# Kernel optimization log

Hardware: AMD Instinct MI355X
Metric: run time of the kernel (lower is better)

The kernel has to match this reference:

```python
import jax, jax.numpy as jnp
import numpy as np

N_NODES = 50000
N_EDGES = 800000
D_IN = 1024
D_OUT = 256
LEAKY_SLOPE = 0.01  # F.leaky_relu default


def setup_inputs() -> dict:
    key = jax.random.key(0)
    k_x, k_w, k_b, k_src, k_dst, k_ew, k_norm = jax.random.split(key, 7)
    x = jax.random.normal(k_x, (N_NODES, D_IN), dtype=jnp.float32)
    # xavier_uniform-style scale for the weight
    limit = np.sqrt(6.0 / (D_IN + D_OUT)).astype(np.float32)
    weight = jax.random.uniform(k_w, (D_IN, D_OUT), dtype=jnp.float32, minval=-limit, maxval=limit)
    stdv = 1.0 / np.sqrt(D_OUT)
    bias = jax.random.uniform(k_b, (D_OUT,), dtype=jnp.float32, minval=-stdv, maxval=stdv)
    src = jax.random.randint(k_src, (N_EDGES,), 0, N_NODES, dtype=jnp.int64)
    dst = jax.random.randint(k_dst, (N_EDGES,), 0, N_NODES, dtype=jnp.int64)
    edge_index = jnp.stack([src, dst], axis=0)  # [2, E]
    edge_weight = jax.random.uniform(k_ew, (N_EDGES,), dtype=jnp.float32)
    norm = jax.random.uniform(k_norm, (N_NODES, 1), dtype=jnp.float32) + 0.5  # avoid div-by-~0
    return {"x": x, "weight": weight, "bias": bias, "edge_index": edge_index,
            "edge_weight": edge_weight, "norm": norm}


def reference(x, weight, bias, edge_index, edge_weight, norm):
    # support = input @ W            [N, D_OUT]
    support = x @ weight
    src = edge_index[0]
    dst = edge_index[1]
    # spmm(adj, support): out[i] = sum_{e: dst_e == i} w_e * support[src_e]
    msgs = support[src] * edge_weight[:, None]            # [E, D_OUT]
    out = jax.ops.segment_sum(msgs, dst, num_segments=x.shape[0])  # [N, D_OUT]
    out = out / norm + bias
    return jax.nn.leaky_relu(out, negative_slope=LEAKY_SLOPE)
```

## Files before the change

kernel.cpp:

```cpp
#include <hip/hip_runtime.h>
#include <hip/hip_bf16.h>

#define N_NODES 50000
#define N_EDGES 800000
#define D_IN    1024
#define D_OUT   256
#define CAP     64
#define LEAKY   0.01f

typedef __attribute__((ext_vector_type(8))) short bf16x8;
typedef __attribute__((ext_vector_type(4))) float f32x4;
typedef __attribute__((ext_vector_type(4))) int   i32x4;
typedef unsigned short u16;

__device__ __forceinline__ u16 f2bfu(float f) {
  uint32_t x = __float_as_uint(f);
  uint32_t r = (x + 0x7FFFu + ((x >> 16) & 1u)) >> 16;
  return (u16)r;
}
__device__ __forceinline__ float bfu2f(u16 u) {
  return __uint_as_float(((uint32_t)u) << 16);
}
__device__ __forceinline__ int swz(int b) { return b ^ (((b >> 7) & 7) << 4); }

__device__ __forceinline__ void gll16(const void* g, void* l) {
  __builtin_amdgcn_global_load_lds(
      (const __attribute__((address_space(1))) uint32_t*)g,
      (__attribute__((address_space(3))) uint32_t*)l, 16, 0, 0);
}

__global__ __launch_bounds__(256) void wconv_kernel(const float* __restrict__ w,
                                                    char* __restrict__ img,
                                                    int* __restrict__ deg) {
  const int t   = blockIdx.x * 256 + threadIdx.x;
  if (t < N_NODES) deg[t] = 0;
  const int t2 = t + 32768;
  if (t2 < N_NODES) deg[t2] = 0;

  const int n   = t & 255;
  const int kc  = (t >> 8) * 8;
  const int kt  = kc >> 6;
  const int kin = kc & 63;
  bf16x8 v;
#pragma unroll
  for (int i = 0; i < 8; ++i) v[i] = (short)f2bfu(w[(size_t)(kc + i) * D_OUT + n]);
  *(bf16x8*)(img + kt * 32768 + swz(n * 128 + kin * 2)) = v;
}

#define BM 64
#define BK 64
#define KSTEPS (D_IN / BK)
#define GEMM_BLOCKS ((N_NODES + BM - 1) / BM)
#define BUILD_BLOCKS 64

__global__ __launch_bounds__(512) void gemm_build_kernel(
    const float* __restrict__ x, const char* __restrict__ img,
    u16* __restrict__ support,
    const int* __restrict__ ei, const float* __restrict__ ew,
    int* __restrict__ deg, int2* __restrict__ csr) {
  __shared__ u16 Wbuf[3][16384];
  __shared__ u16 Xbuf[3][4096];

  if (blockIdx.x < BUILD_BLOCKS) {
    const int t0 = blockIdx.x * 512 + threadIdx.x;
    for (int e = t0; e < N_EDGES; e += BUILD_BLOCKS * 512) {
      const int src = ei[e];
      const int dst = ei[N_EDGES + e];
      const float w = ew[e];
      const int slot = atomicAdd(&deg[dst], 1);
      if (slot < CAP) csr[dst * CAP + slot] = make_int2(src, __float_as_int(w));
    }
    return;
  }

  const int tid  = threadIdx.x;
  const int lane = tid & 63;
  const int wid  = tid >> 6;
  const int wn   = wid & 3;
  const int wm   = wid >> 2;
  const int l15  = lane & 15;
  const int l16  = lane >> 4;
  const int m0   = (blockIdx.x - BUILD_BLOCKS) * BM;

  f32x4 acc[4][2];
#pragma unroll
  for (int i = 0; i < 4; ++i)
#pragma unroll
    for (int j = 0; j < 2; ++j) acc[i][j] = (f32x4)0.0f;

  const int xrow = tid >> 3;
  const int xk8  = (tid & 7) * 8;
  const int xrg  = min(m0 + xrow, N_NODES - 1);
  const float* xp = x + (size_t)xrg * D_IN + xk8;
  const int xw_off = swz(xrow * 128 + xk8 * 2);

  int a_off[2][4], b_off[2][2];
#pragma unroll
  for (int ks = 0; ks < 2; ++ks) {
#pragma unroll
    for (int i = 0; i < 4; ++i)
      a_off[ks][i] = swz((wn * 64 + i * 16 + l15) * 128 + ks * 64 + l16 * 16);
#pragma unroll
    for (int j = 0; j < 2; ++j)
      b_off[ks][j] = swz((wm * 32 + j * 16 + l15) * 128 + ks * 64 + l16 * 16);
  }

  float4 xr[3][2];

#define XLOAD(set, tile) do {                                              \
    const int kcl_ = min((tile), KSTEPS - 1);                              \
    xr[set][0] = *(const float4*)(xp + kcl_ * BK);                         \
    xr[set][1] = *(const float4*)(xp + kcl_ * BK + 4);                     \
  } while (0)

#define WSTAGE(buf, tile) do {                                             \
    const int kcl_ = min((tile), KSTEPS - 1);                              \
    _Pragma("unroll")                                                      \
    for (int r_ = 0; r_ < 4; ++r_)                                         \
      gll16(img + kcl_ * 32768 + r_ * 8192 + tid * 16,                     \
            (char*)&Wbuf[buf][0] + r_ * 8192 + tid * 16);                  \
  } while (0)

#define XCVT(set, buf) do {                                                \
    bf16x8 xv_;                                                            \
    xv_[0] = (short)f2bfu(xr[set][0].x); xv_[1] = (short)f2bfu(xr[set][0].y); \
    xv_[2] = (short)f2bfu(xr[set][0].z); xv_[3] = (short)f2bfu(xr[set][0].w); \
    xv_[4] = (short)f2bfu(xr[set][1].x); xv_[5] = (short)f2bfu(xr[set][1].y); \
    xv_[6] = (short)f2bfu(xr[set][1].z); xv_[7] = (short)f2bfu(xr[set][1].w); \
    *(bf16x8*)((char*)&Xbuf[buf][0] + xw_off) = xv_;                       \
  } while (0)

#define MFMA_TILE(buf) do {                                                \
    _Pragma("unroll")                                                      \
    for (int ks_ = 0; ks_ < 2; ++ks_) {                                    \
      bf16x8 af_[4], bf_[2];                                               \
      _Pragma("unroll")                                                    \
      for (int i_ = 0; i_ < 4; ++i_)                                       \
        af_[i_] = *(const bf16x8*)((const char*)&Wbuf[buf][0] + a_off[ks_][i_]); \
      _Pragma("unroll")                                                    \
      for (int j_ = 0; j_ < 2; ++j_)                                       \
        bf_[j_] = *(const bf16x8*)((const char*)&Xbuf[buf][0] + b_off[ks_][j_]); \
      _Pragma("unroll")                                                    \
      for (int i_ = 0; i_ < 4; ++i_)                                       \
        _Pragma("unroll")                                                  \
        for (int j_ = 0; j_ < 2; ++j_)                                     \
          acc[i_][j_] = __builtin_amdgcn_mfma_f32_16x16x32_bf16(           \
              af_[i_], bf_[j_], acc[i_][j_], 0, 0, 0);                     \
    }                                                                      \
  } while (0)

#define SYNC_COUNTED() do {                                                \
    asm volatile("s_waitcnt vmcnt(6)" ::: "memory");                       \
    __builtin_amdgcn_sched_barrier(0);                                     \
    asm volatile("s_waitcnt lgkmcnt(0)" ::: "memory");                     \
    __builtin_amdgcn_s_barrier();                                          \
  } while (0)

#define BODY(bc, kt) do {                                                  \
    XLOAD((bc + 2) % 3, (kt) + 2);                                         \
    WSTAGE((bc + 2) % 3, (kt) + 2);                                        \
    MFMA_TILE(bc);                                                         \
    XCVT((bc + 1) % 3, (bc + 1) % 3);                                      \
    SYNC_COUNTED();                                                        \
  } while (0)

  XLOAD(0, 0);
  WSTAGE(0, 0);
  XLOAD(1, 1);
  WSTAGE(1, 1);
  XCVT(0, 0);
  SYNC_COUNTED();

  for (int kt = 0; kt < KSTEPS - 1; kt += 3) {
    BODY(0, kt);
    BODY(1, kt + 1);
    BODY(2, kt + 2);
  }
  MFMA_TILE(0);

#undef XLOAD
#undef WSTAGE
#undef XCVT
#undef MFMA_TILE
#undef SYNC_COUNTED
#undef BODY

#pragma unroll
  for (int j = 0; j < 2; ++j) {
    const int m = m0 + wm * 32 + j * 16 + l15;
    if (m < N_NODES) {
#pragma unroll
      for (int i = 0; i < 4; ++i) {
        const int n = wn * 64 + i * 16 + l16 * 4;
        ushort4 o;
        o.x = f2bfu(acc[i][j][0]);
        o.y = f2bfu(acc[i][j][1]);
        o.z = f2bfu(acc[i][j][2]);
        o.w = f2bfu(acc[i][j][3]);
        *(ushort4*)&support[(size_t)m * D_OUT + n] = o;
      }
    }
  }
}

__global__ __launch_bounds__(256) void agg_kernel(const u16* __restrict__ support,
                                                  const int* __restrict__ deg,
                                                  const int2* __restrict__ csr,
                                                  const float* __restrict__ norm,
                                                  const float* __restrict__ bias,
                                                  float* __restrict__ out) {
  const int lane = threadIdx.x & 63;
  const int wid  = threadIdx.x >> 6;
  const int node = blockIdx.x * 4 + wid;
  const int d    = min(deg[node], CAP);
  const int cb   = node * CAP;
  const int ch   = lane * 4;

  float a0 = 0.f, a1 = 0.f, a2 = 0.f, a3 = 0.f;
  int s = 0;

  for (; s + 16 <= d; s += 16) {
    i32x4 q[8];
#pragma unroll
    for (int i = 0; i < 8; ++i)
      q[i] = __builtin_nontemporal_load((const i32x4*)&csr[cb + s + 2 * i]);
    ushort4 v[16];
#pragma unroll
    for (int i = 0; i < 8; ++i) {
      v[2 * i]     = *(const ushort4*)&support[(size_t)q[i][0] * D_OUT + ch];
      v[2 * i + 1] = *(const ushort4*)&support[(size_t)q[i][2] * D_OUT + ch];
    }
#pragma unroll
    for (int i = 0; i < 8; ++i) {
      const float wa = __int_as_float(q[i][1]);
      const float wb = __int_as_float(q[i][3]);
      a0 = fmaf(wa, bfu2f(v[2 * i].x), a0);
      a1 = fmaf(wa, bfu2f(v[2 * i].y), a1);
      a2 = fmaf(wa, bfu2f(v[2 * i].z), a2);
      a3 = fmaf(wa, bfu2f(v[2 * i].w), a3);
      a0 = fmaf(wb, bfu2f(v[2 * i + 1].x), a0);
      a1 = fmaf(wb, bfu2f(v[2 * i + 1].y), a1);
      a2 = fmaf(wb, bfu2f(v[2 * i + 1].z), a2);
      a3 = fmaf(wb, bfu2f(v[2 * i + 1].w), a3);
    }
  }

  for (; s + 8 <= d; s += 8) {
    i32x4 q[4];
#pragma unroll
    for (int i = 0; i < 4; ++i)
      q[i] = __builtin_nontemporal_load((const i32x4*)&csr[cb + s + 2 * i]);
    ushort4 v[8];
#pragma unroll
    for (int i = 0; i < 4; ++i) {
      v[2 * i]     = *(const ushort4*)&support[(size_t)q[i][0] * D_OUT + ch];
      v[2 * i + 1] = *(const ushort4*)&support[(size_t)q[i][2] * D_OUT + ch];
    }
#pragma unroll
    for (int i = 0; i < 4; ++i) {
      const float wa = __int_as_float(q[i][1]);
      const float wb = __int_as_float(q[i][3]);
      a0 = fmaf(wa, bfu2f(v[2 * i].x), a0);
      a1 = fmaf(wa, bfu2f(v[2 * i].y), a1);
      a2 = fmaf(wa, bfu2f(v[2 * i].z), a2);
      a3 = fmaf(wa, bfu2f(v[2 * i].w), a3);
      a0 = fmaf(wb, bfu2f(v[2 * i + 1].x), a0);
      a1 = fmaf(wb, bfu2f(v[2 * i + 1].y), a1);
      a2 = fmaf(wb, bfu2f(v[2 * i + 1].z), a2);
      a3 = fmaf(wb, bfu2f(v[2 * i + 1].w), a3);
    }
  }

  for (; s < d; ++s) {
    const int2  e   = csr[cb + s];
    const float wgt = __int_as_float(e.y);
    const ushort4 v = *(const ushort4*)&support[(size_t)e.x * D_OUT + ch];
    a0 = fmaf(wgt, bfu2f(v.x), a0);
    a1 = fmaf(wgt, bfu2f(v.y), a1);
    a2 = fmaf(wgt, bfu2f(v.z), a2);
    a3 = fmaf(wgt, bfu2f(v.w), a3);
  }

  const float rn = 1.0f / norm[node];
  const float4 b = *(const float4*)&bias[ch];
  float o0 = fmaf(a0, rn, b.x);
  float o1 = fmaf(a1, rn, b.y);
  float o2 = fmaf(a2, rn, b.z);
  float o3 = fmaf(a3, rn, b.w);
  o0 = o0 > 0.f ? o0 : o0 * LEAKY;
  o1 = o1 > 0.f ? o1 : o1 * LEAKY;
  o2 = o2 > 0.f ? o2 : o2 * LEAKY;
  o3 = o3 > 0.f ? o3 : o3 * LEAKY;
  f32x4 ov;
  ov[0] = o0; ov[1] = o1; ov[2] = o2; ov[3] = o3;
  __builtin_nontemporal_store(ov, (f32x4*)&out[(size_t)node * D_OUT + ch]);
}

extern "C" void kernel_launch(void* const* d_in, const int* in_sizes, int n_in,
                              void* d_out, int out_size, void* d_ws, size_t ws_size,
                              hipStream_t stream) {
  const float* x    = (const float*)d_in[0];
  const float* w    = (const float*)d_in[1];
  const float* bias = (const float*)d_in[2];
  const int*   ei   = (const int*)d_in[3];
  const float* ew   = (const float*)d_in[4];
  const float* norm = (const float*)d_in[5];
  float* out = (float*)d_out;

  char* ws = (char*)d_ws;
  u16*   support = (u16*)  (ws);
  char*  img     =         (ws + 25600000);
  int2*  csr     = (int2*) (ws + 26124288);
  int*   deg     = (int*)  (ws + 51724288);

  wconv_kernel<<<128, 256, 0, stream>>>(w, img, deg);
  gemm_build_kernel<<<BUILD_BLOCKS + GEMM_BLOCKS, 512, 0, stream>>>(
      x, img, support, ei, ew, deg, csr);
  agg_kernel<<<N_NODES / 4, 256, 0, stream>>>(support, deg, csr, norm, bias, out);
}
```

Baseline: 168.4 us.

## Enlarge GEMM tile to 256 rows with BK=32 and pairwise-packed swizzled LDS layout

The fused GEMM+CSR-build kernel now gives each block 256 node rows and splits the K dimension into 32-wide steps instead of 64-row blocks with 64-wide steps. Each wave holds a larger 128x64 accumulator tile (8x4 MFMA fragments). The weight image and the LDS buffers use a new packed, swizzled address mapping for the half-width K tiles, and the x loads are marked nontemporal. The bigger tile cuts how often the weight matrix is re-read across blocks and raises MFMA work per LDS read, at the cost of far more accumulator registers, fewer GEMM blocks, a different pipeline phase order and fewer edge-build blocks.

```diff
diff --git a/kernel.cpp b/kernel.cpp
--- a/kernel.cpp
+++ b/kernel.cpp
@@ -22,6 +22,9 @@
   return __uint_as_float(((uint32_t)u) << 16);
 }
 __device__ __forceinline__ int swz(int b) { return b ^ (((b >> 7) & 7) << 4); }
+__device__ __forceinline__ int paddr(int r, int c) {
+  return swz(((r) >> 1) * 128 + ((r) & 1) * 64 + (c));
+}
 
 __device__ __forceinline__ void gll16(const void* g, void* l) {
   __builtin_amdgcn_global_load_lds(
@@ -32,34 +35,32 @@
 __global__ __launch_bounds__(256) void wconv_kernel(const float* __restrict__ w,
                                                     char* __restrict__ img,
                                                     int* __restrict__ deg) {
-  const int t   = blockIdx.x * 256 + threadIdx.x;
+  const int t = blockIdx.x * 256 + threadIdx.x;
   if (t < N_NODES) deg[t] = 0;
   const int t2 = t + 32768;
   if (t2 < N_NODES) deg[t2] = 0;
 
   const int n   = t & 255;
   const int kc  = (t >> 8) * 8;
-  const int kt  = kc >> 6;
-  const int kin = kc & 63;
+  const int kt  = kc >> 5;
+  const int kin = kc & 31;
   bf16x8 v;
 #pragma unroll
   for (int i = 0; i < 8; ++i) v[i] = (short)f2bfu(w[(size_t)(kc + i) * D_OUT + n]);
-  *(bf16x8*)(img + kt * 32768 + swz(n * 128 + kin * 2)) = v;
-}
-
-#define BM 64
-#define BK 64
-#define KSTEPS (D_IN / BK)
-#define GEMM_BLOCKS ((N_NODES + BM - 1) / BM)
-#define BUILD_BLOCKS 64
+  *(bf16x8*)(img + kt * 16384 + paddr(n, kin * 2)) = v;
+}
+
+#define BMg 256
+#define GEMM_BLOCKS ((N_NODES + BMg - 1) / BMg)
+#define BUILD_BLOCKS 60
 
 __global__ __launch_bounds__(512) void gemm_build_kernel(
     const float* __restrict__ x, const char* __restrict__ img,
     u16* __restrict__ support,
     const int* __restrict__ ei, const float* __restrict__ ew,
     int* __restrict__ deg, int2* __restrict__ csr) {
-  __shared__ u16 Wbuf[3][16384];
-  __shared__ u16 Xbuf[3][4096];
+  __shared__ u16 Wbuf[3][8192];
+  __shared__ u16 Xbuf[3][8192];
 
   if (blockIdx.x < BUILD_BLOCKS) {
     const int t0 = blockIdx.x * 512 + threadIdx.x;
@@ -76,127 +77,136 @@
   const int tid  = threadIdx.x;
   const int lane = tid & 63;
   const int wid  = tid >> 6;
-  const int wn   = wid & 3;
-  const int wm   = wid >> 2;
+  const int wn   = wid & 1;
+  const int wm   = wid >> 1;
   const int l15  = lane & 15;
   const int l16  = lane >> 4;
-  const int m0   = (blockIdx.x - BUILD_BLOCKS) * BM;
-
-  f32x4 acc[4][2];
-#pragma unroll
-  for (int i = 0; i < 4; ++i)
-#pragma unroll
-    for (int j = 0; j < 2; ++j) acc[i][j] = (f32x4)0.0f;
-
-  const int xrow = tid >> 3;
-  const int xk8  = (tid & 7) * 8;
+  const int m0   = (blockIdx.x - BUILD_BLOCKS) * BMg;
+
+  f32x4 acc[8][4];
+#pragma unroll
+  for (int i = 0; i < 8; ++i)
+#pragma unroll
+    for (int j = 0; j < 4; ++j) acc[i][j] = (f32x4)0.0f;
+
+  const int xrow = tid >> 1;
+  const int xkc  = (tid & 1) * 16;
   const int xrg  = min(m0 + xrow, N_NODES - 1);
-  const float* xp = x + (size_t)xrg * D_IN + xk8;
-  const int xw_off = swz(xrow * 128 + xk8 * 2);
-
-  int a_off[2][4], b_off[2][2];
-#pragma unroll
-  for (int ks = 0; ks < 2; ++ks) {
-#pragma unroll
-    for (int i = 0; i < 4; ++i)
-      a_off[ks][i] = swz((wn * 64 + i * 16 + l15) * 128 + ks * 64 + l16 * 16);
-#pragma unroll
-    for (int j = 0; j < 2; ++j)
-      b_off[ks][j] = swz((wm * 32 + j * 16 + l15) * 128 + ks * 64 + l16 * 16);
-  }
-
-  float4 xr[3][2];
+  const float* xp = x + (size_t)xrg * D_IN + xkc;
+  const int xw0 = paddr(xrow, xkc * 2);
+  const int xw1 = paddr(xrow, xkc * 2 + 16);
+
+  int a_off[8], b_off[4];
+#pragma unroll
+  for (int nf = 0; nf < 8; ++nf)
+    a_off[nf] = paddr(wn * 128 + nf * 16 + l15, l16 * 16);
+#pragma unroll
+  for (int mf = 0; mf < 4; ++mf)
+    b_off[mf] = paddr(wm * 64 + mf * 16 + l15, l16 * 16);
+
+  f32x4 xr[2][4];
 
 #define XLOAD(set, tile) do {                                              \
-    const int kcl_ = min((tile), KSTEPS - 1);                              \
-    xr[set][0] = *(const float4*)(xp + kcl_ * BK);                         \
-    xr[set][1] = *(const float4*)(xp + kcl_ * BK + 4);                     \
-  } while (0)
-
-#define WSTAGE(buf, tile) do {                                             \
-    const int kcl_ = min((tile), KSTEPS - 1);                              \
+    const int kcl_ = min((tile), 31);                                      \
+    const float* p_ = xp + kcl_ * 32;                                      \
+    xr[set][0] = __builtin_nontemporal_load((const f32x4*)(p_));           \
+    xr[set][1] = __builtin_nontemporal_load((const f32x4*)(p_ + 4));       \
+    xr[set][2] = __builtin_nontemporal_load((const f32x4*)(p_ + 8));       \
+    xr[set][3] = __builtin_nontemporal_load((const f32x4*)(p_ + 12));      \
+  } while (0)
+
+#define GLL(sl, tile) do {                                                 \
+    const int kcl_ = min((tile), 31);                                      \
+    gll16(img + kcl_ * 16384 + tid * 16, (char*)&Wbuf[sl][0] + tid * 16);  \
+    gll16(img + kcl_ * 16384 + 8192 + tid * 16,                            \
+          (char*)&Wbuf[sl][0] + 8192 + tid * 16);                          \
+  } while (0)
+
+#define XCVT(set, sl) do {                                                 \
+    bf16x8 v0_, v1_;                                                       \
+    v0_[0] = (short)f2bfu(xr[set][0][0]); v0_[1] = (short)f2bfu(xr[set][0][1]); \
+    v0_[2] = (short)f2bfu(xr[set][0][2]); v0_[3] = (short)f2bfu(xr[set][0][3]); \
+    v0_[4] = (short)f2bfu(xr[set][1][0]); v0_[5] = (short)f2bfu(xr[set][1][1]); \
+    v0_[6] = (short)f2bfu(xr[set][1][2]); v0_[7] = (short)f2bfu(xr[set][1][3]); \
+    v1_[0] = (short)f2bfu(xr[set][2][0]); v1_[1] = (short)f2bfu(xr[set][2][1]); \
+    v1_[2] = (short)f2bfu(xr[set][2][2]); v1_[3] = (short)f2bfu(xr[set][2][3]); \
+    v1_[4] = (short)f2bfu(xr[set][3][0]); v1_[5] = (short)f2bfu(xr[set][3][1]); \
+    v1_[6] = (short)f2bfu(xr[set][3][2]); v1_[7] = (short)f2bfu(xr[set][3][3]); \
+    *(bf16x8*)((char*)&Xbuf[sl][0] + xw0) = v0_;                           \
+    *(bf16x8*)((char*)&Xbuf[sl][0] + xw1) = v1_;                           \
+  } while (0)
+
+#define MFMA_TILE(sl) do {                                                 \
+    bf16x8 af_[8], bf_[4];                                                 \
     _Pragma("unroll")                                                      \
-    for (int r_ = 0; r_ < 4; ++r_)                                         \
-      gll16(img + kcl_ * 32768 + r_ * 8192 + tid * 16,                     \
-            (char*)&Wbuf[buf][0] + r_ * 8192 + tid * 16);                  \
-  } while (0)
-
-#define XCVT(set, buf) do {                                                \
-    bf16x8 xv_;                                                            \
-    xv_[0] = (short)f2bfu(xr[set][0].x); xv_[1] = (short)f2bfu(xr[set][0].y); \
-    xv_[2] = (short)f2bfu(xr[set][0].z); xv_[3] = (short)f2bfu(xr[set][0].w); \
-    xv_[4] = (short)f2bfu(xr[set][1].x); xv_[5] = (short)f2bfu(xr[set][1].y); \
-    xv_[6] = (short)f2bfu(xr[set][1].z); xv_[7] = (short)f2bfu(xr[set][1].w); \
-    *(bf16x8*)((char*)&Xbuf[buf][0] + xw_off) = xv_;                       \
-  } while (0)
-
-#define MFMA_TILE(buf) do {                                                \
+    for (int nf_ = 0; nf_ < 8; ++nf_)                                      \
+      af_[nf_] = *(const bf16x8*)((const char*)&Wbuf[sl][0] + a_off[nf_]); \
     _Pragma("unroll")                                                      \
-    for (int ks_ = 0; ks_ < 2; ++ks_) {                                    \
-      bf16x8 af_[4], bf_[2];                                               \
+    for (int mf_ = 0; mf_ < 4; ++mf_)                                      \
+      bf_[mf_] = *(const bf16x8*)((const char*)&Xbuf[sl][0] + b_off[mf_]); \
+    _Pragma("unroll")                                                      \
+    for (int nf_ = 0; nf_ < 8; ++nf_)                                      \
       _Pragma("unroll")                                                    \
-      for (int i_ = 0; i_ < 4; ++i_)                                       \
-        af_[i_] = *(const bf16x8*)((const char*)&Wbuf[buf][0] + a_off[ks_][i_]); \
-      _Pragma("unroll")                                                    \
-      for (int j_ = 0; j_ < 2; ++j_)                                       \
-        bf_[j_] = *(const bf16x8*)((const char*)&Xbuf[buf][0] + b_off[ks_][j_]); \
-      _Pragma("unroll")                                                    \
-      for (int i_ = 0; i_ < 4; ++i_)                                       \
-        _Pragma("unroll")                                                  \
-        for (int j_ = 0; j_ < 2; ++j_)                                     \
-          acc[i_][j_] = __builtin_amdgcn_mfma_f32_16x16x32_bf16(           \
-              af_[i_], bf_[j_], acc[i_][j_], 0, 0, 0);                     \
-    }                                                                      \
-  } while (0)
-
-#define SYNC_COUNTED() do {                                                \
+      for (int mf_ = 0; mf_ < 4; ++mf_)                                    \
+        acc[nf_][mf_] = __builtin_amdgcn_mfma_f32_16x16x32_bf16(           \
+            af_[nf_], bf_[mf_], acc[nf_][mf_], 0, 0, 0);                   \
+  } while (0)
+
+#define SYNC() do {                                                        \
     asm volatile("s_waitcnt vmcnt(6)" ::: "memory");                       \
     __builtin_amdgcn_sched_barrier(0);                                     \
     asm volatile("s_waitcnt lgkmcnt(0)" ::: "memory");                     \
     __builtin_amdgcn_s_barrier();                                          \
   } while (0)
 
-#define BODY(bc, kt) do {                                                  \
-    XLOAD((bc + 2) % 3, (kt) + 2);                                         \
-    WSTAGE((bc + 2) % 3, (kt) + 2);                                        \
-    MFMA_TILE(bc);                                                         \
-    XCVT((bc + 1) % 3, (bc + 1) % 3);                                      \
-    SYNC_COUNTED();                                                        \
+#define BODY(sA, sB, sC, eN, eC, kt) do {                                  \
+    MFMA_TILE(sA);                                                         \
+    XCVT(eC, sB);                                                          \
+    XLOAD(eN, (kt) + 2);                                                   \
+    GLL(sC, (kt) + 2);                                                     \
+    SYNC();                                                                \
   } while (0)
 
   XLOAD(0, 0);
-  WSTAGE(0, 0);
+  GLL(0, 0);
   XLOAD(1, 1);
-  WSTAGE(1, 1);
+  GLL(1, 1);
   XCVT(0, 0);
-  SYNC_COUNTED();
-
-  for (int kt = 0; kt < KSTEPS - 1; kt += 3) {
-    BODY(0, kt);
-    BODY(1, kt + 1);
-    BODY(2, kt + 2);
-  }
-  MFMA_TILE(0);
+  asm volatile("s_waitcnt vmcnt(6)" ::: "memory");
+  __builtin_amdgcn_sched_barrier(0);
+  asm volatile("s_waitcnt lgkmcnt(0)" ::: "memory");
+  __builtin_amdgcn_s_barrier();
+
+  for (int kt = 0; kt < 30; kt += 6) {
+    BODY(0, 1, 2, 0, 1, kt);
+    BODY(1, 2, 0, 1, 0, kt + 1);
+    BODY(2, 0, 1, 0, 1, kt + 2);
+    BODY(0, 1, 2, 1, 0, kt + 3);
+    BODY(1, 2, 0, 0, 1, kt + 4);
+    BODY(2, 0, 1, 1, 0, kt + 5);
+  }
+  BODY(0, 1, 2, 0, 1, 30);
+  BODY(1, 2, 0, 1, 0, 31);
 
 #undef XLOAD
-#undef WSTAGE
+#undef GLL
 #undef XCVT
 #undef MFMA_TILE
-#undef SYNC_COUNTED
+#undef SYNC
 #undef BODY
 
 #pragma unroll
-  for (int j = 0; j < 2; ++j) {
-    const int m = m0 + wm * 32 + j * 16 + l15;
+  for (int mf = 0; mf < 4; ++mf) {
+    const int m = m0 + wm * 64 + mf * 16 + l15;
     if (m < N_NODES) {
 #pragma unroll
-      for (int i = 0; i < 4; ++i) {
-        const int n = wn * 64 + i * 16 + l16 * 4;
+      for (int nf = 0; nf < 8; ++nf) {
+        const int n = wn * 128 + nf * 16 + l16 * 4;
         ushort4 o;
-        o.x = f2bfu(acc[i][j][0]);
-        o.y = f2bfu(acc[i][j][1]);
-        o.z = f2bfu(acc[i][j][2]);
-        o.w = f2bfu(acc[i][j][3]);
+        o.x = f2bfu(acc[nf][mf][0]);
+        o.y = f2bfu(acc[nf][mf][1]);
+        o.z = f2bfu(acc[nf][mf][2]);
+        o.w = f2bfu(acc[nf][mf][3]);
         *(ushort4*)&support[(size_t)m * D_OUT + n] = o;
       }
     }
```

Result: slower. 187.2 us (+11.2%).
